# Kernel tuning notes

Hardware: AMD Instinct MI355X
Metric: run time of the kernel (lower is better)

The kernel has to match this reference:

```python
import jax, jax.numpy as jnp
import numpy as np

NUM_CLASSES = 128
EMBED_DIM = 256
HIDDEN = 1024
NUM_LAYERS = 2
BATCH = 64
SEQ = 256


def _gru_layer(x_seq, h0, w_ih, w_hh, b_ih, b_hh):
    # x_seq: [S, B, I], h0: [B, H], w_ih: [3H, I], w_hh: [3H, H]
    gi = jnp.einsum('sbi,gi->sbg', x_seq, w_ih) + b_ih  # precompute input gates [S,B,3H]

    def step(h, gi_t):
        gh = h @ w_hh.T + b_hh
        gir, giz, gin = jnp.split(gi_t, 3, axis=-1)
        ghr, ghz, ghn = jnp.split(gh, 3, axis=-1)
        r = jax.nn.sigmoid(gir + ghr)
        z = jax.nn.sigmoid(giz + ghz)
        n = jnp.tanh(gin + r * ghn)
        h_new = (1.0 - z) * n + z * h
        return h_new, h_new

    hT, out = jax.lax.scan(step, h0, gi)
    return out, hT  # out: [S, B, H]


def setup_inputs() -> dict:
    key = jax.random.key(0)
    ks = jax.random.split(key, 12)
    s_e = 1.0 / np.sqrt(HIDDEN)
    inp = {
        'x': jax.random.randint(ks[0], (BATCH, SEQ), 0, NUM_CLASSES, dtype=jnp.int64),
        'hs': jnp.zeros((NUM_LAYERS, BATCH, HIDDEN), dtype=jnp.float32),
        'embed': jax.random.normal(ks[1], (NUM_CLASSES, EMBED_DIM), dtype=jnp.float32),
        'w_ih0': jax.random.uniform(ks[2], (3 * HIDDEN, EMBED_DIM), minval=-s_e, maxval=s_e, dtype=jnp.float32),
        'w_hh0': jax.random.uniform(ks[3], (3 * HIDDEN, HIDDEN), minval=-s_e, maxval=s_e, dtype=jnp.float32),
        'b_ih0': jax.random.uniform(ks[4], (3 * HIDDEN,), minval=-s_e, maxval=s_e, dtype=jnp.float32),
        'b_hh0': jax.random.uniform(ks[5], (3 * HIDDEN,), minval=-s_e, maxval=s_e, dtype=jnp.float32),
        'w_ih1': jax.random.uniform(ks[6], (3 * HIDDEN, HIDDEN), minval=-s_e, maxval=s_e, dtype=jnp.float32),
        'w_hh1': jax.random.uniform(ks[7], (3 * HIDDEN, HIDDEN), minval=-s_e, maxval=s_e, dtype=jnp.float32),
        'b_ih1': jax.random.uniform(ks[8], (3 * HIDDEN,), minval=-s_e, maxval=s_e, dtype=jnp.float32),
        'b_hh1': jax.random.uniform(ks[9], (3 * HIDDEN,), minval=-s_e, maxval=s_e, dtype=jnp.float32),
        'w_proj': jax.random.uniform(ks[10], (NUM_CLASSES, HIDDEN), minval=-s_e, maxval=s_e, dtype=jnp.float32),
        'b_proj': jax.random.uniform(ks[11], (NUM_CLASSES,), minval=-s_e, maxval=s_e, dtype=jnp.float32),
    }
    return inp


def reference(x, hs, embed, w_ih0, w_hh0, b_ih0, b_hh0, w_ih1, w_hh1, b_ih1, b_hh1, w_proj, b_proj):
    # embedding lookup: [B, S] -> [B, S, E] -> time-major [S, B, E]
    word_embed = embed[x].transpose(1, 0, 2)
    out0, h0T = _gru_layer(word_embed, hs[0], w_ih0, w_hh0, b_ih0, b_hh0)
    out1, h1T = _gru_layer(out0, hs[1], w_ih1, w_hh1, b_ih1, b_hh1)
    # projection: [S, B, H] -> [S, B, C]
    logits = jnp.einsum('sbh,ch->sbc', out1, w_proj) + b_proj
    # permute back to batch-major and flatten: [B*S, C]
    logits = logits.transpose(1, 0, 2).reshape(-1, NUM_CLASSES)
    hT = jnp.stack([h0T, h1T], axis=0)
    return logits, hT
```

## Files before the change

### kernel.cpp

```cpp
#include <hip/hip_runtime.h>
#include <hip/hip_bf16.h>

#define SEQ    256
#define BATCH  64
#define EMB    256
#define HID    1024
#define GATES  3072
#define NCLS   128
#define TCH    16
#define ROWS   (TCH * BATCH)
#define NCH    (SEQ / TCH)
#define MX     (ROWS / 64)

typedef __attribute__((ext_vector_type(8))) short bf16x8;
typedef __attribute__((ext_vector_type(4))) float f32x4;

__device__ inline unsigned short f2bf(float x) {
    union { float f; unsigned int u; } v; v.f = x;
    v.u += 0x7fffu + ((v.u >> 16) & 1u);
    return (unsigned short)(v.u >> 16);
}

__global__ void conv_all(const float* __restrict__ emb, const float* __restrict__ wih0,
                         const float* __restrict__ whh0, const float* __restrict__ wih1,
                         const float* __restrict__ whh1, const float* __restrict__ wproj,
                         const float* __restrict__ hs,
                         unsigned short* __restrict__ embB, unsigned short* __restrict__ wih0B,
                         unsigned short* __restrict__ whh0B, unsigned short* __restrict__ wih1B,
                         unsigned short* __restrict__ whh1B, unsigned short* __restrict__ wprojB,
                         unsigned short* __restrict__ h0b0, unsigned short* __restrict__ h1b0,
                         float* __restrict__ h0f, float* __restrict__ h1f) {
    int i = (blockIdx.x * 256 + threadIdx.x) * 4;
    const float* src; unsigned short* dst; int off;
    if (i < 32768)         { src = emb;   dst = embB;   off = 0; }
    else if (i < 819200)   { src = wih0;  dst = wih0B;  off = 32768; }
    else if (i < 3964928)  { src = whh0;  dst = whh0B;  off = 819200; }
    else if (i < 7110656)  { src = wih1;  dst = wih1B;  off = 3964928; }
    else if (i < 10256384) { src = whh1;  dst = whh1B;  off = 7110656; }
    else if (i < 10387456) { src = wproj; dst = wprojB; off = 10256384; }
    else                   { src = hs;    dst = nullptr; off = 10387456; }
    int k = i - off;
    float4 v = *(const float4*)(src + k);
    if (dst) {
        dst[k + 0] = f2bf(v.x); dst[k + 1] = f2bf(v.y);
        dst[k + 2] = f2bf(v.z); dst[k + 3] = f2bf(v.w);
    } else {
        int kk = k & 65535;
        unsigned short* hb = (k < 65536) ? h0b0 : h1b0;
        float*          hf = (k < 65536) ? h0f  : h1f;
        int b = kk >> 10, j = kk & 1023;
        int bi = ((b >> 4) * 64 + (j >> 4)) * 256 + (b & 15) * 16 + (j & 15);
        hb[bi + 0] = f2bf(v.x); hb[bi + 1] = f2bf(v.y);
        hb[bi + 2] = f2bf(v.z); hb[bi + 3] = f2bf(v.w);
        hf[kk + 0] = v.x; hf[kk + 1] = v.y; hf[kk + 2] = v.z; hf[kk + 3] = v.w;
    }
}

template <int MODE, int KTOT>
__device__ __forceinline__ void gemm_dev(const unsigned short* __restrict__ A,
                                         const unsigned short* __restrict__ Bw,
                                         const float* __restrict__ bias,
                                         float* __restrict__ Cout, int N,
                                         const int* __restrict__ xidx,
                                         const unsigned short* __restrict__ emb,
                                         int row_base, int bx, int by,
                                         unsigned short* smem) {
    const int tid = threadIdx.x;
    const int w = tid >> 6, l = tid & 63;
    const int m0 = bx * 64, n0 = by * 64;
    const int r = l & 15;

    const unsigned short* apt[4];
    const unsigned short* bpt[4];
    int wrA[4], wrB[4];
#pragma unroll
    for (int i = 0; i < 4; ++i) {
        int u = tid + 256 * i;
        int row = u >> 4;
        int ku = u & 15;
        int slot = ku ^ (row & 7);
        if (MODE == 1) {
            int g = row_base + m0 + row;
            apt[i] = emb + (size_t)xidx[(g & 63) * SEQ + (g >> 6)] * KTOT + ku * 8;
        } else {
            apt[i] = A + (size_t)(m0 + row) * KTOT + ku * 8;
        }
        bpt[i] = Bw + (size_t)(n0 + row) * KTOT + ku * 8;
        wrA[i] = row * 128 + slot * 8;
        wrB[i] = 8192 + row * 128 + slot * 8;
    }

    f32x4 acc[4] = {};
    bf16x8 va[4], vb[4];

#pragma unroll
    for (int i = 0; i < 4; ++i) va[i] = *(const bf16x8*)(apt[i]);
#pragma unroll
    for (int i = 0; i < 4; ++i) vb[i] = *(const bf16x8*)(bpt[i]);

    constexpr int NKB = KTOT / 128;
#pragma unroll
    for (int kb = 0; kb < NKB; ++kb) {
#pragma unroll
        for (int i = 0; i < 4; ++i) *(bf16x8*)(smem + wrA[i]) = va[i];
#pragma unroll
        for (int i = 0; i < 4; ++i) *(bf16x8*)(smem + wrB[i]) = vb[i];
        __syncthreads();
        if (kb + 1 < NKB) {
            const int ko = (kb + 1) * 128;
#pragma unroll
            for (int i = 0; i < 4; ++i) va[i] = *(const bf16x8*)(apt[i] + ko);
#pragma unroll
            for (int i = 0; i < 4; ++i) vb[i] = *(const bf16x8*)(bpt[i] + ko);
        }
#pragma unroll
        for (int ks = 0; ks < 4; ++ks) {
            const int slot = (ks * 4 + (l >> 4)) ^ (r & 7);
            bf16x8 a = *(const bf16x8*)(smem + (w * 16 + r) * 128 + slot * 8);
#pragma unroll
            for (int nt = 0; nt < 4; ++nt) {
                bf16x8 b = *(const bf16x8*)(smem + 8192 + (nt * 16 + r) * 128 + slot * 8);
                acc[nt] = __builtin_amdgcn_mfma_f32_16x16x32_bf16(a, b, acc[nt], 0, 0, 0);
            }
        }
        __syncthreads();
    }

    const int la = l & 15, rbase = (l >> 4) * 4;
#pragma unroll
    for (int nt = 0; nt < 4; ++nt) {
        int colg = n0 + nt * 16 + la;
        float bsv = bias[colg];
#pragma unroll
        for (int i = 0; i < 4; ++i) {
            int rowg = m0 + w * 16 + rbase + i;
            float v = acc[nt][i] + bsv;
            if (MODE == 2) {
                int g = row_base + rowg;
                int s = g >> 6, b = g & 63;
                Cout[((size_t)(b * SEQ + s)) * NCLS + colg] = v;
            } else {
                Cout[(size_t)rowg * N + colg] = v;
            }
        }
    }
}

__global__ __launch_bounds__(256)
void gemm_multi(int na, int nb,
                const int* __restrict__ x, const unsigned short* __restrict__ embB,
                const unsigned short* __restrict__ wih0B, const float* __restrict__ bih0,
                float* __restrict__ giA, int rbA,
                const unsigned short* __restrict__ out0b,
                const unsigned short* __restrict__ wih1B, const float* __restrict__ bih1,
                float* __restrict__ giB,
                const unsigned short* __restrict__ out1b,
                const unsigned short* __restrict__ wprojB, const float* __restrict__ bproj,
                float* __restrict__ logits, int rbP) {
    __shared__ unsigned short smem[16384];
    int bid = blockIdx.x;
    if (bid < na) {
        gemm_dev<1, EMB>(nullptr, wih0B, bih0, giA, GATES, x, embB, rbA,
                         bid % MX, bid / MX, smem);
    } else if (bid < na + nb) {
        int b = bid - na;
        gemm_dev<0, HID>(out0b, wih1B, bih1, giB, GATES, nullptr, nullptr, 0,
                         b % MX, b / MX, smem);
    } else {
        int b = bid - na - nb;
        gemm_dev<2, HID>(out1b, wprojB, bproj, logits, NCLS, nullptr, nullptr, rbP,
                         b % MX, b / MX, smem);
    }
}

__device__ __forceinline__ void gru_body(int lb,
        const float* __restrict__ gi, const unsigned short* __restrict__ whb,
        const float* __restrict__ b_hh, float* __restrict__ h_f,
        const unsigned short* __restrict__ hb0, const unsigned short* __restrict__ hb1,
        unsigned short* __restrict__ outseq, int* __restrict__ bar, char* smem) {
    float* sg = (float*)(smem + 32768);

    const int bg = lb >> 6;
    const int jt = lb & 63;
    const int b0 = bg * 16, j0 = jt * 16;
    const int tid = threadIdx.x;
    const int w = tid >> 6, l = tid & 63;

    bf16x8 wreg[32];
    if (w < 3) {
        const unsigned short* wrow = whb + (size_t)(w * HID + j0 + (l & 15)) * HID
                                     + ((l >> 4) * 8);
#pragma unroll
        for (int ks = 0; ks < 32; ++ks) wreg[ks] = *(const bf16x8*)(wrow + ks * 32);
    }

    const int prow = tid >> 4, pcol = tid & 15;
    const int pb = b0 + prow, pj = j0 + pcol;
    float hp = h_f[(size_t)pb * HID + pj];
    const float bhr = b_hh[pj], bhz = b_hh[HID + pj], bhn = b_hh[2 * HID + pj];

    const unsigned short* hbuf[2] = {hb0, hb1};

    const int rr = (tid >> 1) & 15;
    const int swr = (rr & 7) << 4;
    char* hdst = smem + rr * 2048 +
                 ((((tid >> 5) << 5) + ((tid & 1) << 4)) ^ swr);

    for (int t = 0; t < TCH; ++t) {
        const unsigned short* hin = hbuf[t & 1];
        unsigned short* hout = (unsigned short*)hbuf[(t + 1) & 1];

        const float* git = gi + ((size_t)(t * BATCH + pb)) * GATES;
        float gir = git[pj];
        float giz = git[HID + pj];
        float gin = git[2 * HID + pj];

        {
            const unsigned short* s0 = hin + ((size_t)bg << 14) + tid * 8;
            bf16x8 h0v, h1v, h2v, h3v, h4v, h5v, h6v, h7v;
            asm volatile(
                "global_load_dwordx4 %0, %8, off sc0 sc1\n\t"
                "global_load_dwordx4 %1, %9, off sc0 sc1\n\t"
                "global_load_dwordx4 %2, %10, off sc0 sc1\n\t"
                "global_load_dwordx4 %3, %11, off sc0 sc1\n\t"
                "global_load_dwordx4 %4, %12, off sc0 sc1\n\t"
                "global_load_dwordx4 %5, %13, off sc0 sc1\n\t"
                "global_load_dwordx4 %6, %14, off sc0 sc1\n\t"
                "global_load_dwordx4 %7, %15, off sc0 sc1"
                : "=&v"(h0v), "=&v"(h1v), "=&v"(h2v), "=&v"(h3v),
                  "=&v"(h4v), "=&v"(h5v), "=&v"(h6v), "=&v"(h7v)
                : "v"(s0), "v"(s0 + 2048), "v"(s0 + 4096), "v"(s0 + 6144),
                  "v"(s0 + 8192), "v"(s0 + 10240), "v"(s0 + 12288), "v"(s0 + 14336));
            asm volatile("s_waitcnt vmcnt(0)" ::: "memory");
            __builtin_amdgcn_sched_barrier(0);
            *(bf16x8*)(hdst + 0 * 256) = h0v; *(bf16x8*)(hdst + 1 * 256) = h1v;
            *(bf16x8*)(hdst + 2 * 256) = h2v; *(bf16x8*)(hdst + 3 * 256) = h3v;
            *(bf16x8*)(hdst + 4 * 256) = h4v; *(bf16x8*)(hdst + 5 * 256) = h5v;
            *(bf16x8*)(hdst + 6 * 256) = h6v; *(bf16x8*)(hdst + 7 * 256) = h7v;
        }
        __syncthreads();

        if (w < 3) {
            const int r = l & 15;
            const int sw = (r & 7) << 4;
            const int kq = (l >> 4) * 16;
            const int hbyte = r * 2048;
            f32x4 acc = {};
#pragma unroll
            for (int ks = 0; ks < 32; ++ks) {
                bf16x8 a = *(const bf16x8*)(smem + hbyte + ((ks * 64 + kq) ^ sw));
                acc = __builtin_amdgcn_mfma_f32_16x16x32_bf16(a, wreg[ks], acc, 0, 0, 0);
            }
            const int col = l & 15, rbase = (l >> 4) * 4;
#pragma unroll
            for (int i = 0; i < 4; ++i) sg[w * 256 + (rbase + i) * 16 + col] = acc[i];
        }
        __syncthreads();

        float ghr = sg[0 * 256 + tid] + bhr;
        float ghz = sg[1 * 256 + tid] + bhz;
        float ghn = sg[2 * 256 + tid] + bhn;
        float rr2 = 1.f / (1.f + __expf(-(gir + ghr)));
        float zz = 1.f / (1.f + __expf(-(giz + ghz)));
        float nn = tanhf(gin + rr2 * ghn);
        hp = (1.f - zz) * nn + zz * hp;
        unsigned short hb = f2bf(hp);
        outseq[((size_t)(t * BATCH + pb)) * HID + pj] = hb;

        *(unsigned short*)(smem + tid * 2) = hb;
        __syncthreads();

        if (tid < 32) {
            bf16x8 pk = *(const bf16x8*)(smem + tid * 16);
            unsigned short* dstp = hout + ((size_t)(bg * 64 + jt) << 8) + tid * 8;
            asm volatile(
                "global_store_dwordx4 %0, %1, off sc0 sc1\n\t"
                "s_waitcnt vmcnt(0)"
                :: "v"(dstp), "v"(pk) : "memory");
        }

        if (t < TCH - 1) {
            if (tid == 0) {
                __hip_atomic_store(bar + (((bg << 6) | jt) << 4), t + 1,
                                   __ATOMIC_RELAXED, __HIP_MEMORY_SCOPE_AGENT);
            }
            if (tid < 64) {
                const int* f = bar + (((bg << 6) | tid) << 4);
                while (!__all(__hip_atomic_load(f, __ATOMIC_RELAXED,
                                                __HIP_MEMORY_SCOPE_AGENT) > t)) {
                    __builtin_amdgcn_s_sleep(1);
                }
            }
            __syncthreads();
        }
    }

    h_f[(size_t)pb * HID + pj] = hp;
}

__global__ __launch_bounds__(256, 2)
void mega(int g0, int g1, int na, int nb, int np,
          const float* __restrict__ gi0, const unsigned short* __restrict__ wh0,
          const float* __restrict__ bh0, float* __restrict__ h0f,
          unsigned short* __restrict__ h0p, unsigned short* __restrict__ h0q,
          unsigned short* __restrict__ out0, int* __restrict__ bar0,
          const float* __restrict__ gi1, const unsigned short* __restrict__ wh1,
          const float* __restrict__ bh1, float* __restrict__ h1f,
          unsigned short* __restrict__ h1p, unsigned short* __restrict__ h1q,
          unsigned short* __restrict__ out1, int* __restrict__ bar1,
          const int* __restrict__ x, const unsigned short* __restrict__ embB,
          const unsigned short* __restrict__ wih0B, const float* __restrict__ bih0,
          float* __restrict__ giA_nxt, int rbA,
          const unsigned short* __restrict__ out0_prev,
          const unsigned short* __restrict__ wih1B, const float* __restrict__ bih1,
          float* __restrict__ giB_nxt,
          const unsigned short* __restrict__ out1_old,
          const unsigned short* __restrict__ wprojB, const float* __restrict__ bproj,
          float* __restrict__ logits, int rbP) {
    __shared__ char smem[35840];
    const int bid = blockIdx.x;
    const int ng = g0 + g1;
    if (bid < ng) {
        if (bid < g0)
            gru_body(bid, gi0, wh0, bh0, h0f, h0p, h0q, out0, bar0, smem);
        else
            gru_body(bid - g0, gi1, wh1, bh1, h1f, h1p, h1q, out1, bar1, smem);
    } else {
        int b2 = bid - ng;
        if (b2 < na) {
            gemm_dev<1, EMB>(nullptr, wih0B, bih0, giA_nxt, GATES, x, embB, rbA,
                             b2 % MX, b2 / MX, (unsigned short*)smem);
        } else if (b2 < na + nb) {
            int b = b2 - na;
            gemm_dev<0, HID>(out0_prev, wih1B, bih1, giB_nxt, GATES, nullptr, nullptr, 0,
                             b % MX, b / MX, (unsigned short*)smem);
        } else {
            int b = b2 - na - nb;
            gemm_dev<2, HID>(out1_old, wprojB, bproj, logits, NCLS, nullptr, nullptr, rbP,
                             b % MX, b / MX, (unsigned short*)smem);
        }
    }
}

extern "C" void kernel_launch(void* const* d_in, const int* in_sizes, int n_in,
                              void* d_out, int out_size, void* d_ws, size_t ws_size,
                              hipStream_t stream) {
    const int*   x      = (const int*)d_in[0];
    const float* hs     = (const float*)d_in[1];
    const float* emb    = (const float*)d_in[2];
    const float* w_ih0  = (const float*)d_in[3];
    const float* w_hh0  = (const float*)d_in[4];
    const float* b_ih0  = (const float*)d_in[5];
    const float* b_hh0  = (const float*)d_in[6];
    const float* w_ih1  = (const float*)d_in[7];
    const float* w_hh1  = (const float*)d_in[8];
    const float* b_ih1  = (const float*)d_in[9];
    const float* b_hh1  = (const float*)d_in[10];
    const float* w_proj = (const float*)d_in[11];
    const float* b_proj = (const float*)d_in[12];

    float* logits = (float*)d_out;
    float* hT     = logits + (size_t)SEQ * BATCH * NCLS;

    const size_t GI_BYTES = (size_t)ROWS * GATES * 4;
    const bool big = ws_size >= ((size_t)82 << 20);

    char* p = (char*)d_ws;
    float* giA[2]; float* giB[2];
    giA[0] = (float*)p; p += GI_BYTES;
    giA[1] = big ? (float*)p : giA[0]; if (big) p += GI_BYTES;
    giB[0] = (float*)p; p += GI_BYTES;
    giB[1] = big ? (float*)p : giB[0]; if (big) p += GI_BYTES;
    float* h0f = (float*)p;                     p += 65536 * 4;
    float* h1f = (float*)p;                     p += 65536 * 4;
    unsigned short* h0b0 = (unsigned short*)p;  p += 65536 * 2;
    unsigned short* h0b1 = (unsigned short*)p;  p += 65536 * 2;
    unsigned short* h1b0 = (unsigned short*)p;  p += 65536 * 2;
    unsigned short* h1b1 = (unsigned short*)p;  p += 65536 * 2;
    unsigned short* out0b[2];
    out0b[0] = (unsigned short*)p;              p += (size_t)ROWS * HID * 2;
    out0b[1] = big ? (unsigned short*)p : out0b[0]; if (big) p += (size_t)ROWS * HID * 2;
    unsigned short* out1b[2];
    out1b[0] = (unsigned short*)p;              p += (size_t)ROWS * HID * 2;
    out1b[1] = (unsigned short*)p;              p += (size_t)ROWS * HID * 2;
    unsigned short* embB  = (unsigned short*)p; p += (size_t)NCLS * EMB * 2;
    unsigned short* wih0B = (unsigned short*)p; p += (size_t)GATES * EMB * 2;
    unsigned short* whh0B = (unsigned short*)p; p += (size_t)GATES * HID * 2;
    unsigned short* wih1B = (unsigned short*)p; p += (size_t)GATES * HID * 2;
    unsigned short* whh1B = (unsigned short*)p; p += (size_t)GATES * HID * 2;
    unsigned short* wprojB = (unsigned short*)p; p += (size_t)NCLS * HID * 2;
    int* bar = (int*)p;                         p += (size_t)32 * 4096 * 4;

    hipMemsetAsync(bar, 0, (size_t)32 * 4096 * 4, stream);

    conv_all<<<10272, 256, 0, stream>>>(emb, w_ih0, w_hh0, w_ih1, w_hh1, w_proj, hs,
                                        embB, wih0B, whh0B, wih1B, whh1B, wprojB,
                                        h0b0, h1b0, h0f, h1f);

    if (big) {
        gemm_multi<<<768, 256, 0, stream>>>(768, 0,
            x, embB, wih0B, b_ih0, giA[0], 0,
            out0b[0], wih1B, b_ih1, giB[0],
            out1b[0], wprojB, b_proj, logits, 0);

        for (int k = 0; k < 18; ++k) {
            int g0 = (k <= 15) ? 256 : 0;
            int g1 = (k >= 2) ? 256 : 0;
            int na = (k <= 14) ? 768 : 0;
            int nb = (k >= 1 && k <= 16) ? 768 : 0;
            int np = (k >= 3) ? 32 : 0;
            int m = k - 2, n = k - 1, q = k - 3;
            mega<<<g0 + g1 + na + nb + np, 256, 0, stream>>>(
                g0, g1, na, nb, np,
                giA[k & 1], whh0B, b_hh0, h0f, h0b0, h0b1, out0b[k & 1],
                bar + (size_t)(k & 15) * 4096,
                giB[m & 1], whh1B, b_hh1, h1f, h1b0, h1b1, out1b[m & 1],
                bar + (size_t)(16 + (m & 15)) * 4096,
                x, embB, wih0B, b_ih0, giA[(k + 1) & 1], (k + 1) * ROWS,
                out0b[n & 1], wih1B, b_ih1, giB[n & 1],
                out1b[q & 1], wprojB, b_proj, logits, q * ROWS);
        }

        gemm_multi<<<32, 256, 0, stream>>>(0, 0,
            x, embB, wih0B, b_ih0, giA[0], 0,
            out0b[0], wih1B, b_ih1, giB[0],
            out1b[1], wprojB, b_proj, logits, 15 * ROWS);
    } else {
        for (int c = 0; c < NCH; ++c) {
            int na = 768;
            int nb = (c >= 1) ? 768 : 0;
            int np = (c >= 2) ? 32 : 0;
            gemm_multi<<<na + nb + np, 256, 0, stream>>>(na, nb,
                x, embB, wih0B, b_ih0, giA[0], c * ROWS,
                out0b[0], wih1B, b_ih1, giB[0],
                out1b[(c - 2) & 1], wprojB, b_proj, logits,
                (c >= 2) ? (c - 2) * ROWS : 0);

            int g1 = (c >= 1) ? 256 : 0;
            int c1 = (c >= 1) ? c - 1 : 0;
            mega<<<256 + g1, 256, 0, stream>>>(256, g1, 0, 0, 0,
                giA[0], whh0B, b_hh0, h0f, h0b0, h0b1, out0b[0],
                bar + (size_t)c * 4096,
                giB[0], whh1B, b_hh1, h1f, h1b0, h1b1, out1b[c1 & 1],
                bar + (size_t)(16 + c1) * 4096,
                x, embB, wih0B, b_ih0, giA[0], 0,
                out0b[0], wih1B, b_ih1, giB[0],
                out1b[0], wprojB, b_proj, logits, 0);
        }
        gemm_multi<<<768 + 32, 256, 0, stream>>>(0, 768,
            x, embB, wih0B, b_ih0, giA[0], 0,
            out0b[0], wih1B, b_ih1, giB[0],
            out1b[0], wprojB, b_proj, logits, 14 * ROWS);
        mega<<<256, 256, 0, stream>>>(0, 256, 0, 0, 0,
            giA[0], whh0B, b_hh0, h0f, h0b0, h0b1, out0b[0], bar,
            giB[0], whh1B, b_hh1, h1f, h1b0, h1b1, out1b[1],
            bar + (size_t)31 * 4096,
            x, embB, wih0B, b_ih0, giA[0], 0,
            out0b[0], wih1B, b_ih1, giB[0],
            out1b[0], wprojB, b_proj, logits, 0);
        gemm_multi<<<32, 256, 0, stream>>>(0, 0,
            x, embB, wih0B, b_ih0, giA[0], 0,
            out0b[0], wih1B, b_ih1, giB[0],
            out1b[1], wprojB, b_proj, logits, 15 * ROWS);
    }

    hipMemcpyAsync(hT, h0f, 65536 * 4, hipMemcpyDeviceToDevice, stream);
    hipMemcpyAsync(hT + 65536, h1f, 65536 * 4, hipMemcpyDeviceToDevice, stream);
}
```

Before: 1.527 ms.

## Tag hidden-state words with step sequence to replace flag-barrier polling

```diff
diff --git a/kernel.cpp b/kernel.cpp
--- a/kernel.cpp
+++ b/kernel.cpp
@@ -14,6 +14,8 @@
 
 typedef __attribute__((ext_vector_type(8))) short bf16x8;
 typedef __attribute__((ext_vector_type(4))) float f32x4;
+typedef __attribute__((ext_vector_type(4))) unsigned int u32x4;
+typedef __attribute__((ext_vector_type(2))) unsigned int u32x2;
 
 __device__ inline unsigned short f2bf(float x) {
     union { float f; unsigned int u; } v; v.f = x;
@@ -28,7 +30,7 @@
                          unsigned short* __restrict__ embB, unsigned short* __restrict__ wih0B,
                          unsigned short* __restrict__ whh0B, unsigned short* __restrict__ wih1B,
                          unsigned short* __restrict__ whh1B, unsigned short* __restrict__ wprojB,
-                         unsigned short* __restrict__ h0b0, unsigned short* __restrict__ h1b0,
+                         unsigned int* __restrict__ h0b0, unsigned int* __restrict__ h1b0,
                          float* __restrict__ h0f, float* __restrict__ h1f) {
     int i = (blockIdx.x * 256 + threadIdx.x) * 4;
     const float* src; unsigned short* dst; int off;
@@ -46,12 +48,14 @@
         dst[k + 2] = f2bf(v.z); dst[k + 3] = f2bf(v.w);
     } else {
         int kk = k & 65535;
-        unsigned short* hb = (k < 65536) ? h0b0 : h1b0;
-        float*          hf = (k < 65536) ? h0f  : h1f;
+        unsigned int* hb = (k < 65536) ? h0b0 : h1b0;
+        float*        hf = (k < 65536) ? h0f  : h1f;
         int b = kk >> 10, j = kk & 1023;
         int bi = ((b >> 4) * 64 + (j >> 4)) * 256 + (b & 15) * 16 + (j & 15);
-        hb[bi + 0] = f2bf(v.x); hb[bi + 1] = f2bf(v.y);
-        hb[bi + 2] = f2bf(v.z); hb[bi + 3] = f2bf(v.w);
+        hb[bi + 0] = (unsigned int)f2bf(v.x) << 16;
+        hb[bi + 1] = (unsigned int)f2bf(v.y) << 16;
+        hb[bi + 2] = (unsigned int)f2bf(v.z) << 16;
+        hb[bi + 3] = (unsigned int)f2bf(v.w) << 16;
         hf[kk + 0] = v.x; hf[kk + 1] = v.y; hf[kk + 2] = v.z; hf[kk + 3] = v.w;
     }
 }
@@ -173,10 +177,36 @@
     }
 }
 
-__device__ __forceinline__ void gru_body(int lb,
+#define LOAD16                                                                \
+    asm volatile(                                                             \
+        "global_load_dwordx4 %0, %16, off sc0 sc1\n\t"                        \
+        "global_load_dwordx4 %1, %16, off offset:16 sc0 sc1\n\t"              \
+        "global_load_dwordx4 %2, %16, off offset:32 sc0 sc1\n\t"              \
+        "global_load_dwordx4 %3, %16, off offset:48 sc0 sc1\n\t"              \
+        "global_load_dwordx4 %4, %16, off offset:64 sc0 sc1\n\t"              \
+        "global_load_dwordx4 %5, %16, off offset:80 sc0 sc1\n\t"              \
+        "global_load_dwordx4 %6, %16, off offset:96 sc0 sc1\n\t"              \
+        "global_load_dwordx4 %7, %16, off offset:112 sc0 sc1\n\t"             \
+        "global_load_dwordx4 %8, %16, off offset:128 sc0 sc1\n\t"             \
+        "global_load_dwordx4 %9, %16, off offset:144 sc0 sc1\n\t"             \
+        "global_load_dwordx4 %10, %16, off offset:160 sc0 sc1\n\t"            \
+        "global_load_dwordx4 %11, %16, off offset:176 sc0 sc1\n\t"            \
+        "global_load_dwordx4 %12, %16, off offset:192 sc0 sc1\n\t"            \
+        "global_load_dwordx4 %13, %16, off offset:208 sc0 sc1\n\t"            \
+        "global_load_dwordx4 %14, %16, off offset:224 sc0 sc1\n\t"            \
+        "global_load_dwordx4 %15, %16, off offset:240 sc0 sc1\n\t"            \
+        "s_waitcnt vmcnt(0)"                                                  \
+        : "=&v"(u0), "=&v"(u1), "=&v"(u2), "=&v"(u3),                         \
+          "=&v"(u4), "=&v"(u5), "=&v"(u6), "=&v"(u7),                         \
+          "=&v"(u8), "=&v"(u9), "=&v"(u10), "=&v"(u11),                       \
+          "=&v"(u12), "=&v"(u13), "=&v"(u14), "=&v"(u15)                      \
+        : "v"(hbase)                                                          \
+        : "memory")
+
+__device__ __forceinline__ void gru_body(int lb, int sbase,
         const float* __restrict__ gi, const unsigned short* __restrict__ whb,
         const float* __restrict__ b_hh, float* __restrict__ h_f,
-        const unsigned short* __restrict__ hb0, const unsigned short* __restrict__ hb1,
+        unsigned int* __restrict__ hb0, unsigned int* __restrict__ hb1,
         unsigned short* __restrict__ outseq, int* __restrict__ bar, char* smem) {
     float* sg = (float*)(smem + 32768);
 
@@ -199,45 +229,51 @@
     float hp = h_f[(size_t)pb * HID + pj];
     const float bhr = b_hh[pj], bhz = b_hh[HID + pj], bhn = b_hh[2 * HID + pj];
 
-    const unsigned short* hbuf[2] = {hb0, hb1};
-
-    const int rr = (tid >> 1) & 15;
-    const int swr = (rr & 7) << 4;
-    char* hdst = smem + rr * 2048 +
-                 ((((tid >> 5) << 5) + ((tid & 1) << 4)) ^ swr);
+    unsigned int* hbuf[2] = {hb0, hb1};
+
+    const int rb = (tid & 3) * 4;
+    const int jb2 = (tid >> 2) * 32;
+
+#define CHK(V) ((V[0] ^ sexp) | (V[1] ^ sexp) | (V[2] ^ sexp) | (V[3] ^ sexp))
+#define PUT(K, V) do {                                                        \
+        int r_ = rb + ((K) >> 2);                                             \
+        u32x2 pk_;                                                            \
+        pk_[0] = (V[0] >> 16) | (V[1] & 0xffff0000u);                         \
+        pk_[1] = (V[2] >> 16) | (V[3] & 0xffff0000u);                         \
+        *(u32x2*)(smem + r_ * 2048 +                                          \
+                  ((jb2 + ((K) & 3) * 8) ^ ((r_ & 7) << 4))) = pk_;           \
+    } while (0)
 
     for (int t = 0; t < TCH; ++t) {
-        const unsigned short* hin = hbuf[t & 1];
-        unsigned short* hout = (unsigned short*)hbuf[(t + 1) & 1];
+        const unsigned int* hin = hbuf[t & 1];
+        unsigned int* hout = hbuf[(t + 1) & 1];
+        const unsigned int sexp = (unsigned int)(sbase + t) & 0xffffu;
 
         const float* git = gi + ((size_t)(t * BATCH + pb)) * GATES;
         float gir = git[pj];
         float giz = git[HID + pj];
         float gin = git[2 * HID + pj];
 
-        {
-            const unsigned short* s0 = hin + ((size_t)bg << 14) + tid * 8;
-            bf16x8 h0v, h1v, h2v, h3v, h4v, h5v, h6v, h7v;
-            asm volatile(
-                "global_load_dwordx4 %0, %8, off sc0 sc1\n\t"
-                "global_load_dwordx4 %1, %9, off sc0 sc1\n\t"
-                "global_load_dwordx4 %2, %10, off sc0 sc1\n\t"
-                "global_load_dwordx4 %3, %11, off sc0 sc1\n\t"
-                "global_load_dwordx4 %4, %12, off sc0 sc1\n\t"
-                "global_load_dwordx4 %5, %13, off sc0 sc1\n\t"
-                "global_load_dwordx4 %6, %14, off sc0 sc1\n\t"
-                "global_load_dwordx4 %7, %15, off sc0 sc1"
-                : "=&v"(h0v), "=&v"(h1v), "=&v"(h2v), "=&v"(h3v),
-                  "=&v"(h4v), "=&v"(h5v), "=&v"(h6v), "=&v"(h7v)
-                : "v"(s0), "v"(s0 + 2048), "v"(s0 + 4096), "v"(s0 + 6144),
-                  "v"(s0 + 8192), "v"(s0 + 10240), "v"(s0 + 12288), "v"(s0 + 14336));
-            asm volatile("s_waitcnt vmcnt(0)" ::: "memory");
-            __builtin_amdgcn_sched_barrier(0);
-            *(bf16x8*)(hdst + 0 * 256) = h0v; *(bf16x8*)(hdst + 1 * 256) = h1v;
-            *(bf16x8*)(hdst + 2 * 256) = h2v; *(bf16x8*)(hdst + 3 * 256) = h3v;
-            *(bf16x8*)(hdst + 4 * 256) = h4v; *(bf16x8*)(hdst + 5 * 256) = h5v;
-            *(bf16x8*)(hdst + 6 * 256) = h6v; *(bf16x8*)(hdst + 7 * 256) = h7v;
-        }
+        const unsigned int* hbase = hin + ((size_t)bg << 14) + (size_t)tid * 64;
+        u32x4 u0, u1, u2, u3, u4, u5, u6, u7, u8, u9, u10, u11, u12, u13, u14, u15;
+        LOAD16;
+        unsigned int bad = CHK(u0) | CHK(u1) | CHK(u2) | CHK(u3) |
+                           CHK(u4) | CHK(u5) | CHK(u6) | CHK(u7) |
+                           CHK(u8) | CHK(u9) | CHK(u10) | CHK(u11) |
+                           CHK(u12) | CHK(u13) | CHK(u14) | CHK(u15);
+        if (!__all((bad & 0xffffu) == 0)) {
+            const int* f = bar + (((bg << 6) | l) << 4);
+            while (!__all(__hip_atomic_load(f, __ATOMIC_RELAXED,
+                                            __HIP_MEMORY_SCOPE_AGENT) > t - 1)) {
+                __builtin_amdgcn_s_sleep(1);
+            }
+            LOAD16;
+        }
+
+        PUT(0, u0);  PUT(1, u1);  PUT(2, u2);  PUT(3, u3);
+        PUT(4, u4);  PUT(5, u5);  PUT(6, u6);  PUT(7, u7);
+        PUT(8, u8);  PUT(9, u9);  PUT(10, u10); PUT(11, u11);
+        PUT(12, u12); PUT(13, u13); PUT(14, u14); PUT(15, u15);
         __syncthreads();
 
         if (w < 3) {
@@ -267,46 +303,39 @@
         unsigned short hb = f2bf(hp);
         outseq[((size_t)(t * BATCH + pb)) * HID + pj] = hb;
 
-        *(unsigned short*)(smem + tid * 2) = hb;
-        __syncthreads();
-
-        if (tid < 32) {
-            bf16x8 pk = *(const bf16x8*)(smem + tid * 16);
-            unsigned short* dstp = hout + ((size_t)(bg * 64 + jt) << 8) + tid * 8;
+        ((unsigned int*)smem)[tid] =
+            ((unsigned int)hb << 16) | ((unsigned int)(sbase + t + 1) & 0xffffu);
+        __syncthreads();
+
+        if (tid < 64) {
+            u32x4 pk = *(const u32x4*)(smem + tid * 16);
+            unsigned int* dstp = hout + ((size_t)(bg * 64 + jt) << 8) + tid * 4;
             asm volatile(
                 "global_store_dwordx4 %0, %1, off sc0 sc1\n\t"
                 "s_waitcnt vmcnt(0)"
                 :: "v"(dstp), "v"(pk) : "memory");
-        }
-
-        if (t < TCH - 1) {
-            if (tid == 0) {
+            if (tid == 0 && t < TCH - 1) {
                 __hip_atomic_store(bar + (((bg << 6) | jt) << 4), t + 1,
                                    __ATOMIC_RELAXED, __HIP_MEMORY_SCOPE_AGENT);
             }
-            if (tid < 64) {
-                const int* f = bar + (((bg << 6) | tid) << 4);
-                while (!__all(__hip_atomic_load(f, __ATOMIC_RELAXED,
-                                                __HIP_MEMORY_SCOPE_AGENT) > t)) {
-                    __builtin_amdgcn_s_sleep(1);
-                }
-            }
-            __syncthreads();
-        }
+        }
+        __syncthreads();
     }
 
     h_f[(size_t)pb * HID + pj] = hp;
+#undef CHK
+#undef PUT
 }
 
 __global__ __launch_bounds__(256, 2)
-void mega(int g0, int g1, int na, int nb, int np,
+void mega(int g0, int g1, int na, int nb, int np, int sb0, int sb1,
           const float* __restrict__ gi0, const unsigned short* __restrict__ wh0,
           const float* __restrict__ bh0, float* __restrict__ h0f,
-          unsigned short* __restrict__ h0p, unsigned short* __restrict__ h0q,
+          unsigned int* __restrict__ h0p, unsigned int* __restrict__ h0q,
           unsigned short* __restrict__ out0, int* __restrict__ bar0,
           const float* __restrict__ gi1, const unsigned short* __restrict__ wh1,
           const float* __restrict__ bh1, float* __restrict__ h1f,
-          unsigned short* __restrict__ h1p, unsigned short* __restrict__ h1q,
+          unsigned int* __restrict__ h1p, unsigned int* __restrict__ h1q,
           unsigned short* __restrict__ out1, int* __restrict__ bar1,
           const int* __restrict__ x, const unsigned short* __restrict__ embB,
           const unsigned short* __restrict__ wih0B, const float* __restrict__ bih0,
@@ -322,9 +351,9 @@
     const int ng = g0 + g1;
     if (bid < ng) {
         if (bid < g0)
-            gru_body(bid, gi0, wh0, bh0, h0f, h0p, h0q, out0, bar0, smem);
+            gru_body(bid, sb0, gi0, wh0, bh0, h0f, h0p, h0q, out0, bar0, smem);
         else
-            gru_body(bid - g0, gi1, wh1, bh1, h1f, h1p, h1q, out1, bar1, smem);
+            gru_body(bid - g0, sb1, gi1, wh1, bh1, h1f, h1p, h1q, out1, bar1, smem);
     } else {
         int b2 = bid - ng;
         if (b2 < na) {
@@ -373,10 +402,10 @@
     giB[1] = big ? (float*)p : giB[0]; if (big) p += GI_BYTES;
     float* h0f = (float*)p;                     p += 65536 * 4;
     float* h1f = (float*)p;                     p += 65536 * 4;
-    unsigned short* h0b0 = (unsigned short*)p;  p += 65536 * 2;
-    unsigned short* h0b1 = (unsigned short*)p;  p += 65536 * 2;
-    unsigned short* h1b0 = (unsigned short*)p;  p += 65536 * 2;
-    unsigned short* h1b1 = (unsigned short*)p;  p += 65536 * 2;
+    unsigned int* h0b0 = (unsigned int*)p;      p += 65536 * 4;
+    unsigned int* h0b1 = (unsigned int*)p;      p += 65536 * 4;
+    unsigned int* h1b0 = (unsigned int*)p;      p += 65536 * 4;
+    unsigned int* h1b1 = (unsigned int*)p;      p += 65536 * 4;
     unsigned short* out0b[2];
     out0b[0] = (unsigned short*)p;              p += (size_t)ROWS * HID * 2;
     out0b[1] = big ? (unsigned short*)p : out0b[0]; if (big) p += (size_t)ROWS * HID * 2;
@@ -411,7 +440,7 @@
             int np = (k >= 3) ? 32 : 0;
             int m = k - 2, n = k - 1, q = k - 3;
             mega<<<g0 + g1 + na + nb + np, 256, 0, stream>>>(
-                g0, g1, na, nb, np,
+                g0, g1, na, nb, np, k * TCH, (m >= 0 ? m : 0) * TCH,
                 giA[k & 1], whh0B, b_hh0, h0f, h0b0, h0b1, out0b[k & 1],
                 bar + (size_t)(k & 15) * 4096,
                 giB[m & 1], whh1B, b_hh1, h1f, h1b0, h1b1, out1b[m & 1],
@@ -438,7 +467,7 @@
 
             int g1 = (c >= 1) ? 256 : 0;
             int c1 = (c >= 1) ? c - 1 : 0;
-            mega<<<256 + g1, 256, 0, stream>>>(256, g1, 0, 0, 0,
+            mega<<<256 + g1, 256, 0, stream>>>(256, g1, 0, 0, 0, c * TCH, c1 * TCH,
                 giA[0], whh0B, b_hh0, h0f, h0b0, h0b1, out0b[0],
                 bar + (size_t)c * 4096,
                 giB[0], whh1B, b_hh1, h1f, h1b0, h1b1, out1b[c1 & 1],
@@ -451,7 +480,7 @@
             x, embB, wih0B, b_ih0, giA[0], 0,
             out0b[0], wih1B, b_ih1, giB[0],
             out1b[0], wprojB, b_proj, logits, 14 * ROWS);
-        mega<<<256, 256, 0, stream>>>(0, 256, 0, 0, 0,
+        mega<<<256, 256, 0, stream>>>(0, 256, 0, 0, 0, 0, 15 * TCH,
             giA[0], whh0B, b_hh0, h0f, h0b0, h0b1, out0b[0], bar,
             giB[0], whh1B, b_hh1, h1f, h1b0, h1b1, out1b[1],
             bar + (size_t)31 * 4096,
```

New measurement: 5.653 ms. 3.7x slower.
